# Performance work log

Hardware: AMD Instinct MI355X
Metric: run time of the kernel (lower is better)

Reference implementation:

```python
import jax, jax.numpy as jnp
import numpy as np

U, I, D, K, B, NNEG = 500000, 500000, 64, 32, 8192, 128
W1, W2, W3, W4 = 1e-6, 1.0, 1e-6, 1.0
NEG_WEIGHT, GAMMA, LAMBDA = 200.0, 1e-4, 2.5


def setup_inputs() -> dict:
    key = jax.random.key(0)
    ks = jax.random.split(key, 14)
    return {
        "users": jax.random.randint(ks[0], (B,), 0, U),
        "pos_items": jax.random.randint(ks[1], (B,), 0, I),
        "neg_items": jax.random.randint(ks[2], (B, NNEG), 0, I),
        "rpkms": jax.random.normal(ks[3], (B,), dtype=jnp.float32),
        "user_emb": jax.random.normal(ks[4], (U, D), dtype=jnp.float32) * 1e-2,
        "item_emb": jax.random.normal(ks[5], (I, D), dtype=jnp.float32) * 1e-2,
        "beta_uD": jax.random.uniform(ks[6], (U,), dtype=jnp.float32),
        "beta_iD": jax.random.uniform(ks[7], (I,), dtype=jnp.float32),
        "ii_neighbor_mat": jax.random.randint(ks[8], (I, K), 0, I),
        "ii_constraint_mat": jax.random.uniform(ks[9], (I, K), dtype=jnp.float32),
        "mse_u_w": jax.random.normal(ks[10], (D, D), dtype=jnp.float32) * 0.05,
        "mse_u_b": jnp.zeros((D,), jnp.float32),
        "mse_i_w": jax.random.normal(ks[11], (D, D), dtype=jnp.float32) * 0.05,
        "mse_i_b": jnp.zeros((D,), jnp.float32),
        "fc1_w1": jax.random.normal(ks[12], (D, 2 * D), dtype=jnp.float32) * 0.05,
        "fc1_b1": jnp.zeros((D,), jnp.float32),
        "fc1_w2": jax.random.normal(ks[13], (1, D), dtype=jnp.float32) * 0.05,
        "fc1_b2": jnp.zeros((1,), jnp.float32),
    }


def reference(users, pos_items, neg_items, rpkms, user_emb, item_emb,
              beta_uD, beta_iD, ii_neighbor_mat, ii_constraint_mat,
              mse_u_w, mse_u_b, mse_i_w, mse_i_b,
              fc1_w1, fc1_b1, fc1_w2, fc1_b2):
    sp = jax.nn.softplus  # -log(sigmoid(x)) == softplus(-x)

    ue = user_emb[users]            # [B, D]
    pe = item_emb[pos_items]        # [B, D]
    ne = item_emb[neg_items]        # [B, N, D]

    # ---- omegas ----
    pos_w = W1 + W2 * beta_uD[users] * beta_iD[pos_items]          # [B]
    neg_w = W3 + W4 * beta_uD[users][:, None] * beta_iD[neg_items]  # [B, N]

    # ---- cal_loss_L (weighted BCE with logits) ----
    pos_scores = jnp.sum(ue * pe, axis=-1)                  # [B]
    neg_scores = jnp.einsum('bd,bnd->bn', ue, ne)           # [B, N]
    pos_loss = pos_w * sp(-pos_scores)                      # label 1
    neg_loss = jnp.mean(neg_w * sp(neg_scores), axis=-1)    # label 0, mean over negs
    loss_L = jnp.mean(pos_loss + neg_loss * NEG_WEIGHT)

    # ---- norm_loss over all learned parameters ----
    params = (user_emb, item_emb, mse_u_w, mse_u_b, mse_i_w, mse_i_b,
              fc1_w1, fc1_b1, fc1_w2, fc1_b2)
    norm = GAMMA * 0.5 * sum(jnp.sum(p * p) for p in params)

    # ---- cal_loss_I: gather item-item neighbors of pos_items ----
    nbr = item_emb[ii_neighbor_mat[pos_items]]              # [B, K, D]
    sim = ii_constraint_mat[pos_items]                      # [B, K]
    loss_I = LAMBDA * jnp.mean(sim * sp(-jnp.einsum('bd,bkd->bk', ue, nbr)))

    # ---- mse_loss ----
    feat_u = ue @ mse_u_w.T + mse_u_b
    feat_i = pe @ mse_i_w.T + mse_i_b
    pred = jnp.sum(feat_u * feat_i, axis=-1)
    mse = jnp.mean((pred - rpkms) ** 2)

    total = loss_L + norm + loss_I + mse
    zero = jnp.float32(0.0)  # torch returns torch.tensor(0.0) as 4th element
    return jnp.stack([total, loss_L, loss_I, zero, mse, norm])
```

## Files before the change

kernel.cpp:

```cpp
#include <hip/hip_runtime.h>
#include <math.h>

#define UU 500000
#define II 500000
#define DD 64
#define KK 32
#define BB 8192
#define NNEG 128

#define NORMB 1024
#define GATHB (BB / 4)

typedef float v4f __attribute__((ext_vector_type(4)));

__device__ __forceinline__ float softplus_f(float x) {
    return fmaxf(x, 0.0f) + log1pf(expf(-fabsf(x)));
}

__device__ __forceinline__ float waveReduceSum(float v) {
#pragma unroll
    for (int off = 32; off > 0; off >>= 1) v += __shfl_xor(v, off, 64);
    return v;
}

__global__ __launch_bounds__(256) void fused_kernel(
    const int* __restrict__ users, const int* __restrict__ pos_items,
    const int* __restrict__ neg_items,
    const float* __restrict__ user_emb, const float* __restrict__ item_emb,
    const float* __restrict__ beta_uD, const float* __restrict__ beta_iD,
    const int* __restrict__ ii_nbr, const float* __restrict__ ii_con,
    const float* __restrict__ mse_u_w, const float* __restrict__ mse_u_b,
    const float* __restrict__ mse_i_w, const float* __restrict__ mse_i_b,
    const float* __restrict__ fc1_w1, const float* __restrict__ fc1_b1,
    const float* __restrict__ fc1_w2, const float* __restrict__ fc1_b2,
    float* __restrict__ acc)
{
    const int wave = threadIdx.x >> 6;
    const int lane = threadIdx.x & 63;
    __shared__ float red[4];

    if (blockIdx.x < NORMB) {
        const size_t tid = (size_t)blockIdx.x * blockDim.x + threadIdx.x;
        const size_t st  = (size_t)NORMB * 256;
        const size_t n4  = (size_t)UU * DD / 4;
        float s0 = 0.f, s1 = 0.f, s2 = 0.f, s3 = 0.f;

        {
            const v4f* a = (const v4f*)user_emb;
            size_t i = tid;
            for (; i + 3 * st < n4; i += 4 * st) {
                v4f x0 = __builtin_nontemporal_load(&a[i]);
                v4f x1 = __builtin_nontemporal_load(&a[i + st]);
                v4f x2 = __builtin_nontemporal_load(&a[i + 2 * st]);
                v4f x3 = __builtin_nontemporal_load(&a[i + 3 * st]);
                s0 += x0.x*x0.x + x0.y*x0.y + x0.z*x0.z + x0.w*x0.w;
                s1 += x1.x*x1.x + x1.y*x1.y + x1.z*x1.z + x1.w*x1.w;
                s2 += x2.x*x2.x + x2.y*x2.y + x2.z*x2.z + x2.w*x2.w;
                s3 += x3.x*x3.x + x3.y*x3.y + x3.z*x3.z + x3.w*x3.w;
            }
            for (; i < n4; i += st) {
                v4f x = __builtin_nontemporal_load(&a[i]);
                s0 += x.x*x.x + x.y*x.y + x.z*x.z + x.w*x.w;
            }
        }
        {
            const v4f* c = (const v4f*)item_emb;
            size_t i = tid;
            for (; i + 3 * st < n4; i += 4 * st) {
                v4f x0 = c[i];
                v4f x1 = c[i + st];
                v4f x2 = c[i + 2 * st];
                v4f x3 = c[i + 3 * st];
                s0 += x0.x*x0.x + x0.y*x0.y + x0.z*x0.z + x0.w*x0.w;
                s1 += x1.x*x1.x + x1.y*x1.y + x1.z*x1.z + x1.w*x1.w;
                s2 += x2.x*x2.x + x2.y*x2.y + x2.z*x2.z + x2.w*x2.w;
                s3 += x3.x*x3.x + x3.y*x3.y + x3.z*x3.z + x3.w*x3.w;
            }
            for (; i < n4; i += st) {
                v4f x = c[i];
                s0 += x.x*x.x + x.y*x.y + x.z*x.z + x.w*x.w;
            }
        }
        float s = (s0 + s1) + (s2 + s3);
        for (size_t i = tid; i < (size_t)DD * DD; i += st)
            s += mse_u_w[i] * mse_u_w[i] + mse_i_w[i] * mse_i_w[i];
        for (size_t i = tid; i < (size_t)DD * 2 * DD; i += st)
            s += fc1_w1[i] * fc1_w1[i];
        for (size_t i = tid; i < (size_t)DD; i += st)
            s += mse_u_b[i] * mse_u_b[i] + mse_i_b[i] * mse_i_b[i]
               + fc1_b1[i] * fc1_b1[i] + fc1_w2[i] * fc1_w2[i];
        if (tid == 0) s += fc1_b2[0] * fc1_b2[0];

        s = waveReduceSum(s);
        if (lane == 0) red[wave] = s;
        __syncthreads();
        if (threadIdx.x == 0)
            atomicAdd(&acc[2], red[0] + red[1] + red[2] + red[3]);
        return;
    }

    const int b = (blockIdx.x - NORMB) * 4 + wave;
    float accL = 0.f, accI = 0.f;

    const int u_idx = users[b];
    const int p_idx = pos_items[b];
    const float u_reg = user_emb[(size_t)u_idx * DD + lane];
    const float bu = beta_uD[u_idx];

    __shared__ float sU[4][DD];
    sU[wave][lane] = u_reg;

    const int q  = lane & 3;
    const int li = lane >> 2;

    float4 uv[4];
#pragma unroll
    for (int j = 0; j < 4; ++j)
        uv[j] = *(const float4*)&sU[wave][j * 16 + q * 4];

    {
        const float p = item_emb[(size_t)p_idx * DD + lane];
        const float pos_dot = waveReduceSum(u_reg * p);
        if (lane == 0)
            accL += (1e-6f + bu * beta_iD[p_idx]) * softplus_f(-pos_dot);
    }

    const int i0 = neg_items[(size_t)b * NNEG + lane];
    const int i1 = neg_items[(size_t)b * NNEG + 64 + lane];
    const float bn0 = beta_iD[i0];
    const float bn1 = beta_iD[i1];

    const float negscale4 = 0.25f * (200.0f / (float)NNEG);

#pragma unroll
    for (int g = 0; g < 2; ++g) {
        const int   srcI = g ? i1 : i0;
        const float srcB = g ? bn1 : bn0;
        float4 vb[4][4];
        float  bi4[4];
#pragma unroll
        for (int t = 0; t < 4; ++t) {
            const int n = t * 16 + li;
            const int idx = __shfl(srcI, n, 64);
            bi4[t] = __shfl(srcB, n, 64);
            const float* row = item_emb + (size_t)idx * DD + q * 4;
#pragma unroll
            for (int j = 0; j < 4; ++j)
                vb[t][j] = *(const float4*)(row + j * 16);
        }
#pragma unroll
        for (int t = 0; t < 4; ++t) {
            float dot = 0.f;
#pragma unroll
            for (int j = 0; j < 4; ++j) {
                dot = fmaf(vb[t][j].x, uv[j].x, dot);
                dot = fmaf(vb[t][j].y, uv[j].y, dot);
                dot = fmaf(vb[t][j].z, uv[j].z, dot);
                dot = fmaf(vb[t][j].w, uv[j].w, dot);
            }
            dot += __shfl_xor(dot, 1, 64);
            dot += __shfl_xor(dot, 2, 64);
            accL += negscale4 * (1e-6f + bu * bi4[t]) * softplus_f(dot);
        }
    }

    int nbv = 0; float simv = 0.f;
    if (lane < KK) {
        nbv  = ii_nbr[(size_t)p_idx * KK + lane];
        simv = ii_con[(size_t)p_idx * KK + lane];
    }
    {
        float4 vb[2][4];
        float  sk2[2];
#pragma unroll
        for (int t = 0; t < 2; ++t) {
            const int n = t * 16 + li;
            const int idx = __shfl(nbv, n, 64);
            sk2[t] = __shfl(simv, n, 64);
            const float* row = item_emb + (size_t)idx * DD + q * 4;
#pragma unroll
            for (int j = 0; j < 4; ++j)
                vb[t][j] = *(const float4*)(row + j * 16);
        }
#pragma unroll
        for (int t = 0; t < 2; ++t) {
            float dot = 0.f;
#pragma unroll
            for (int j = 0; j < 4; ++j) {
                dot = fmaf(vb[t][j].x, uv[j].x, dot);
                dot = fmaf(vb[t][j].y, uv[j].y, dot);
                dot = fmaf(vb[t][j].z, uv[j].z, dot);
                dot = fmaf(vb[t][j].w, uv[j].w, dot);
            }
            dot += __shfl_xor(dot, 1, 64);
            dot += __shfl_xor(dot, 2, 64);
            accI += 0.25f * sk2[t] * softplus_f(-dot);
        }
    }

    accL = waveReduceSum(accL);
    accI = waveReduceSum(accI);
    __shared__ float redL[4], redI[4];
    if (lane == 0) { redL[wave] = accL; redI[wave] = accI; }
    __syncthreads();
    if (threadIdx.x == 0) {
        atomicAdd(&acc[0], redL[0] + redL[1] + redL[2] + redL[3]);
        atomicAdd(&acc[1], redI[0] + redI[1] + redI[2] + redI[3]);
    }
}

__global__ __launch_bounds__(256) void mse_kernel(
    const int* __restrict__ users, const int* __restrict__ pos_items,
    const float* __restrict__ rpkms,
    const float* __restrict__ user_emb, const float* __restrict__ item_emb,
    const float* __restrict__ mse_u_w, const float* __restrict__ mse_u_b,
    const float* __restrict__ mse_i_w, const float* __restrict__ mse_i_b,
    float* __restrict__ acc)
{
    __shared__ float sWu[DD * (DD + 1)];
    __shared__ float sWi[DD * (DD + 1)];
    __shared__ float sBu[DD], sBi[DD];
    __shared__ float sUe[4][DD], sPe[4][DD];

    for (int i = threadIdx.x; i < DD * DD; i += blockDim.x) {
        const int r = i >> 6, c = i & 63;
        sWu[r * (DD + 1) + c] = mse_u_w[i];
        sWi[r * (DD + 1) + c] = mse_i_w[i];
    }
    if (threadIdx.x < DD) {
        sBu[threadIdx.x] = mse_u_b[threadIdx.x];
        sBi[threadIdx.x] = mse_i_b[threadIdx.x];
    }

    const int wave = threadIdx.x >> 6;
    const int lane = threadIdx.x & 63;
    const int b = blockIdx.x * 4 + wave;
    sUe[wave][lane] = user_emb[(size_t)users[b] * DD + lane];
    sPe[wave][lane] = item_emb[(size_t)pos_items[b] * DD + lane];
    __syncthreads();

    float fu = sBu[lane];
    float fi = sBi[lane];
#pragma unroll 8
    for (int d = 0; d < DD; ++d) {
        fu += sUe[wave][d] * sWu[lane * (DD + 1) + d];
        fi += sPe[wave][d] * sWi[lane * (DD + 1) + d];
    }
    const float pred = waveReduceSum(fu * fi);
    if (lane == 0) {
        const float diff = pred - rpkms[b];
        atomicAdd(&acc[3], diff * diff);
    }
}

__global__ void finalize_kernel(const float* __restrict__ acc, float* __restrict__ out)
{
    if (threadIdx.x == 0) {
        const float loss_L = acc[0] / (float)BB;
        const float loss_I = 2.5f * acc[1] / (float)(BB * KK);
        const float mse    = acc[3] / (float)BB;
        const float norm   = 1e-4f * 0.5f * acc[2];
        const float total  = loss_L + norm + loss_I + mse;
        out[0] = total;
        out[1] = loss_L;
        out[2] = loss_I;
        out[3] = 0.0f;
        out[4] = mse;
        out[5] = norm;
    }
}

extern "C" void kernel_launch(void* const* d_in, const int* in_sizes, int n_in,
                              void* d_out, int out_size, void* d_ws, size_t ws_size,
                              hipStream_t stream)
{
    const int*   users      = (const int*)  d_in[0];
    const int*   pos_items  = (const int*)  d_in[1];
    const int*   neg_items  = (const int*)  d_in[2];
    const float* rpkms      = (const float*)d_in[3];
    const float* user_emb   = (const float*)d_in[4];
    const float* item_emb   = (const float*)d_in[5];
    const float* beta_uD    = (const float*)d_in[6];
    const float* beta_iD    = (const float*)d_in[7];
    const int*   ii_nbr     = (const int*)  d_in[8];
    const float* ii_con     = (const float*)d_in[9];
    const float* mse_u_w    = (const float*)d_in[10];
    const float* mse_u_b    = (const float*)d_in[11];
    const float* mse_i_w    = (const float*)d_in[12];
    const float* mse_i_b    = (const float*)d_in[13];
    const float* fc1_w1     = (const float*)d_in[14];
    const float* fc1_b1     = (const float*)d_in[15];
    const float* fc1_w2     = (const float*)d_in[16];
    const float* fc1_b2     = (const float*)d_in[17];

    float* acc = (float*)d_ws;
    hipMemsetAsync(d_ws, 0, 4 * sizeof(float), stream);

    fused_kernel<<<NORMB + GATHB, 256, 0, stream>>>(users, pos_items, neg_items,
                                                    user_emb, item_emb, beta_uD, beta_iD,
                                                    ii_nbr, ii_con,
                                                    mse_u_w, mse_u_b, mse_i_w, mse_i_b,
                                                    fc1_w1, fc1_b1, fc1_w2, fc1_b2, acc);

    mse_kernel<<<BB / 4, 256, 0, stream>>>(users, pos_items, rpkms,
                                           user_emb, item_emb,
                                           mse_u_w, mse_u_b, mse_i_w, mse_i_b, acc);

    finalize_kernel<<<1, 64, 0, stream>>>(acc, (float*)d_out);
}
```

Baseline: 531.5 us.

## Gather negatives from a bf16 item table built during the norm pass

```diff
diff --git a/kernel.cpp b/kernel.cpp
--- a/kernel.cpp
+++ b/kernel.cpp
@@ -8,9 +8,6 @@
 #define BB 8192
 #define NNEG 128
 
-#define NORMB 1024
-#define GATHB (BB / 4)
-
 typedef float v4f __attribute__((ext_vector_type(4)));
 
 __device__ __forceinline__ float softplus_f(float x) {
@@ -23,7 +20,225 @@
     return v;
 }
 
-__global__ __launch_bounds__(256) void fused_kernel(
+__device__ __forceinline__ unsigned int bf16pack2(float lo, float hi) {
+    unsigned int ul = __float_as_uint(lo);
+    ul += 0x7FFFu + ((ul >> 16) & 1u);
+    unsigned int uh = __float_as_uint(hi);
+    uh += 0x7FFFu + ((uh >> 16) & 1u);
+    return (ul >> 16) | (uh & 0xFFFF0000u);
+}
+
+__global__ __launch_bounds__(256) void norm_convert_kernel(
+    const float* __restrict__ user_emb, const float* __restrict__ item_emb,
+    unsigned int* __restrict__ bfit,
+    const float* __restrict__ mse_u_w, const float* __restrict__ mse_u_b,
+    const float* __restrict__ mse_i_w, const float* __restrict__ mse_i_b,
+    const float* __restrict__ fc1_w1, const float* __restrict__ fc1_b1,
+    const float* __restrict__ fc1_w2, const float* __restrict__ fc1_b2,
+    float* __restrict__ acc)
+{
+    const size_t tid = (size_t)blockIdx.x * blockDim.x + threadIdx.x;
+    const size_t st  = (size_t)gridDim.x * blockDim.x;
+    float s = 0.f;
+
+    {
+        const size_t npair = (size_t)II * DD / 8;
+        const v4f* it4 = (const v4f*)item_emb;
+        uint4* out4 = (uint4*)bfit;
+        for (size_t k = tid; k < npair; k += st) {
+            v4f a = __builtin_nontemporal_load(&it4[2 * k]);
+            v4f b = __builtin_nontemporal_load(&it4[2 * k + 1]);
+            s += a.x*a.x + a.y*a.y + a.z*a.z + a.w*a.w;
+            s += b.x*b.x + b.y*b.y + b.z*b.z + b.w*b.w;
+            uint4 w;
+            w.x = bf16pack2(a.x, a.y);
+            w.y = bf16pack2(a.z, a.w);
+            w.z = bf16pack2(b.x, b.y);
+            w.w = bf16pack2(b.z, b.w);
+            out4[k] = w;
+        }
+    }
+    {
+        const size_t n4 = (size_t)UU * DD / 4;
+        const v4f* a = (const v4f*)user_emb;
+        for (size_t i = tid; i < n4; i += st) {
+            v4f x = __builtin_nontemporal_load(&a[i]);
+            s += x.x*x.x + x.y*x.y + x.z*x.z + x.w*x.w;
+        }
+    }
+    for (size_t i = tid; i < (size_t)DD * DD; i += st)
+        s += mse_u_w[i] * mse_u_w[i] + mse_i_w[i] * mse_i_w[i];
+    for (size_t i = tid; i < (size_t)DD * 2 * DD; i += st)
+        s += fc1_w1[i] * fc1_w1[i];
+    for (size_t i = tid; i < (size_t)DD; i += st)
+        s += mse_u_b[i] * mse_u_b[i] + mse_i_b[i] * mse_i_b[i]
+           + fc1_b1[i] * fc1_b1[i] + fc1_w2[i] * fc1_w2[i];
+    if (tid == 0) s += fc1_b2[0] * fc1_b2[0];
+
+    s = waveReduceSum(s);
+    __shared__ float red[4];
+    if ((threadIdx.x & 63) == 0) red[threadIdx.x >> 6] = s;
+    __syncthreads();
+    if (threadIdx.x == 0)
+        atomicAdd(&acc[2], red[0] + red[1] + red[2] + red[3]);
+}
+
+__global__ __launch_bounds__(256) void gather_mse_kernel(
+    const int* __restrict__ users, const int* __restrict__ pos_items,
+    const int* __restrict__ neg_items, const float* __restrict__ rpkms,
+    const float* __restrict__ user_emb, const float* __restrict__ item_emb,
+    const unsigned int* __restrict__ bfit,
+    const float* __restrict__ beta_uD, const float* __restrict__ beta_iD,
+    const int* __restrict__ ii_nbr, const float* __restrict__ ii_con,
+    const float* __restrict__ mse_u_w, const float* __restrict__ mse_u_b,
+    const float* __restrict__ mse_i_w, const float* __restrict__ mse_i_b,
+    float* __restrict__ acc)
+{
+    const int wave = threadIdx.x >> 6;
+    const int lane = threadIdx.x & 63;
+    const int b = blockIdx.x * 4 + wave;
+
+    const int u_idx = users[b];
+    const int p_idx = pos_items[b];
+    const float u_reg = user_emb[(size_t)u_idx * DD + lane];
+    const float p_reg = item_emb[(size_t)p_idx * DD + lane];
+    const float bu = beta_uD[u_idx];
+
+    __shared__ float sU[4][DD];
+    __shared__ float sP[4][DD];
+    sU[wave][lane] = u_reg;
+    sP[wave][lane] = p_reg;
+
+    const int q  = lane & 3;
+    const int li = lane >> 2;
+
+    float4 uv[4], pv[4];
+#pragma unroll
+    for (int j = 0; j < 4; ++j) {
+        uv[j] = *(const float4*)&sU[wave][q * 16 + j * 4];
+        pv[j] = *(const float4*)&sP[wave][q * 16 + j * 4];
+    }
+
+    float accL = 0.f, accI = 0.f, accM = 0.f;
+
+    {
+        const float pos_dot = waveReduceSum(u_reg * p_reg);
+        if (lane == 0)
+            accL += (1e-6f + bu * beta_iD[p_idx]) * softplus_f(-pos_dot);
+    }
+
+    const int i0 = neg_items[(size_t)b * NNEG + lane];
+    const int i1 = neg_items[(size_t)b * NNEG + 64 + lane];
+    const float bn0 = beta_iD[i0];
+    const float bn1 = beta_iD[i1];
+    int nbv = 0; float simv = 0.f;
+    if (lane < KK) {
+        nbv  = ii_nbr[(size_t)p_idx * KK + lane];
+        simv = ii_con[(size_t)p_idx * KK + lane];
+    }
+
+    const float negscale4 = 0.25f * (200.0f / (float)NNEG);
+
+    uint4 rg[3][2];
+    float rw[3];
+
+#define PREP(g, slot)                                                          \
+    {                                                                          \
+        int idx; float w;                                                      \
+        if ((g) < 4)      { idx = __shfl(i0, (g) * 16 + li, 64);               \
+                            w   = __shfl(bn0, (g) * 16 + li, 64); }            \
+        else if ((g) < 8) { idx = __shfl(i1, ((g) - 4) * 16 + li, 64);         \
+                            w   = __shfl(bn1, ((g) - 4) * 16 + li, 64); }      \
+        else              { idx = __shfl(nbv, ((g) - 8) * 16 + li, 64);        \
+                            w   = __shfl(simv, ((g) - 8) * 16 + li, 64); }     \
+        const uint4* row = (const uint4*)(bfit + (size_t)idx * (DD / 2));      \
+        rg[slot][0] = row[q * 2];                                              \
+        rg[slot][1] = row[q * 2 + 1];                                          \
+        rw[slot] = w;                                                          \
+    }
+
+#define DOT8(wv, ua, ub, d)                                                    \
+    {                                                                          \
+        d = fmaf(__uint_as_float((wv).x << 16), ua.x, d);                      \
+        d = fmaf(__uint_as_float((wv).x & 0xFFFF0000u), ua.y, d);              \
+        d = fmaf(__uint_as_float((wv).y << 16), ua.z, d);                      \
+        d = fmaf(__uint_as_float((wv).y & 0xFFFF0000u), ua.w, d);              \
+        d = fmaf(__uint_as_float((wv).z << 16), ub.x, d);                      \
+        d = fmaf(__uint_as_float((wv).z & 0xFFFF0000u), ub.y, d);              \
+        d = fmaf(__uint_as_float((wv).w << 16), ub.z, d);                      \
+        d = fmaf(__uint_as_float((wv).w & 0xFFFF0000u), ub.w, d);              \
+    }
+
+#define CONSUME(g, slot)                                                       \
+    {                                                                          \
+        float dot = 0.f;                                                       \
+        DOT8(rg[slot][0], uv[0], uv[1], dot);                                  \
+        DOT8(rg[slot][1], uv[2], uv[3], dot);                                  \
+        dot += __shfl_xor(dot, 1, 64);                                         \
+        dot += __shfl_xor(dot, 2, 64);                                         \
+        if ((g) < 8) accL += negscale4 * (1e-6f + bu * rw[slot]) * softplus_f(dot); \
+        else         accI += 0.25f * rw[slot] * softplus_f(-dot);              \
+    }
+
+    PREP(0, 0); PREP(1, 1); PREP(2, 2);
+    CONSUME(0, 0); PREP(3, 0);
+    CONSUME(1, 1); PREP(4, 1);
+    CONSUME(2, 2); PREP(5, 2);
+    CONSUME(3, 0); PREP(6, 0);
+    CONSUME(4, 1); PREP(7, 1);
+    CONSUME(5, 2); PREP(8, 2);
+    CONSUME(6, 0); PREP(9, 0);
+    CONSUME(7, 1);
+    CONSUME(8, 2);
+    CONSUME(9, 0);
+#undef PREP
+#undef DOT8
+#undef CONSUME
+
+    {
+        float pq = 0.f;
+#pragma unroll
+        for (int g = 0; g < 4; ++g) {
+            const int r = g * 16 + li;
+            const float* wur = mse_u_w + r * DD + q * 16;
+            const float* wir = mse_i_w + r * DD + q * 16;
+            float fu = 0.f, fi = 0.f;
+#pragma unroll
+            for (int j = 0; j < 4; ++j) {
+                const float4 a = *(const float4*)(wur + j * 4);
+                fu = fmaf(a.x, uv[j].x, fu); fu = fmaf(a.y, uv[j].y, fu);
+                fu = fmaf(a.z, uv[j].z, fu); fu = fmaf(a.w, uv[j].w, fu);
+                const float4 c = *(const float4*)(wir + j * 4);
+                fi = fmaf(c.x, pv[j].x, fi); fi = fmaf(c.y, pv[j].y, fi);
+                fi = fmaf(c.z, pv[j].z, fi); fi = fmaf(c.w, pv[j].w, fi);
+            }
+            fu += __shfl_xor(fu, 1, 64); fu += __shfl_xor(fu, 2, 64);
+            fi += __shfl_xor(fi, 1, 64); fi += __shfl_xor(fi, 2, 64);
+            fu += mse_u_b[r];
+            fi += mse_i_b[r];
+            pq += fu * fi;
+        }
+        const float pred = waveReduceSum(pq) * 0.25f;
+        if (lane == 0) {
+            const float diff = pred - rpkms[b];
+            accM += diff * diff;
+        }
+    }
+
+    accL = waveReduceSum(accL);
+    accI = waveReduceSum(accI);
+    __shared__ float redL[4], redI[4], redM[4];
+    if (lane == 0) { redL[wave] = accL; redI[wave] = accI; redM[wave] = accM; }
+    __syncthreads();
+    if (threadIdx.x == 0) {
+        atomicAdd(&acc[0], redL[0] + redL[1] + redL[2] + redL[3]);
+        atomicAdd(&acc[1], redI[0] + redI[1] + redI[2] + redI[3]);
+        atomicAdd(&acc[3], redM[0] + redM[1] + redM[2] + redM[3]);
+    }
+}
+
+#define NORMB 1024
+__global__ __launch_bounds__(256) void fb_fused_kernel(
     const int* __restrict__ users, const int* __restrict__ pos_items,
     const int* __restrict__ neg_items,
     const float* __restrict__ user_emb, const float* __restrict__ item_emb,
@@ -43,45 +258,15 @@
         const size_t tid = (size_t)blockIdx.x * blockDim.x + threadIdx.x;
         const size_t st  = (size_t)NORMB * 256;
         const size_t n4  = (size_t)UU * DD / 4;
-        float s0 = 0.f, s1 = 0.f, s2 = 0.f, s3 = 0.f;
-
-        {
-            const v4f* a = (const v4f*)user_emb;
-            size_t i = tid;
-            for (; i + 3 * st < n4; i += 4 * st) {
-                v4f x0 = __builtin_nontemporal_load(&a[i]);
-                v4f x1 = __builtin_nontemporal_load(&a[i + st]);
-                v4f x2 = __builtin_nontemporal_load(&a[i + 2 * st]);
-                v4f x3 = __builtin_nontemporal_load(&a[i + 3 * st]);
-                s0 += x0.x*x0.x + x0.y*x0.y + x0.z*x0.z + x0.w*x0.w;
-                s1 += x1.x*x1.x + x1.y*x1.y + x1.z*x1.z + x1.w*x1.w;
-                s2 += x2.x*x2.x + x2.y*x2.y + x2.z*x2.z + x2.w*x2.w;
-                s3 += x3.x*x3.x + x3.y*x3.y + x3.z*x3.z + x3.w*x3.w;
-            }
-            for (; i < n4; i += st) {
-                v4f x = __builtin_nontemporal_load(&a[i]);
-                s0 += x.x*x.x + x.y*x.y + x.z*x.z + x.w*x.w;
-            }
-        }
-        {
-            const v4f* c = (const v4f*)item_emb;
-            size_t i = tid;
-            for (; i + 3 * st < n4; i += 4 * st) {
-                v4f x0 = c[i];
-                v4f x1 = c[i + st];
-                v4f x2 = c[i + 2 * st];
-                v4f x3 = c[i + 3 * st];
-                s0 += x0.x*x0.x + x0.y*x0.y + x0.z*x0.z + x0.w*x0.w;
-                s1 += x1.x*x1.x + x1.y*x1.y + x1.z*x1.z + x1.w*x1.w;
-                s2 += x2.x*x2.x + x2.y*x2.y + x2.z*x2.z + x2.w*x2.w;
-                s3 += x3.x*x3.x + x3.y*x3.y + x3.z*x3.z + x3.w*x3.w;
-            }
-            for (; i < n4; i += st) {
-                v4f x = c[i];
-                s0 += x.x*x.x + x.y*x.y + x.z*x.z + x.w*x.w;
-            }
-        }
-        float s = (s0 + s1) + (s2 + s3);
+        float s = 0.f;
+        const v4f* a = (const v4f*)user_emb;
+        for (size_t i = tid; i < n4; i += st) {
+            v4f x = a[i]; s += x.x*x.x + x.y*x.y + x.z*x.z + x.w*x.w;
+        }
+        const v4f* c = (const v4f*)item_emb;
+        for (size_t i = tid; i < n4; i += st) {
+            v4f x = c[i]; s += x.x*x.x + x.y*x.y + x.z*x.z + x.w*x.w;
+        }
         for (size_t i = tid; i < (size_t)DD * DD; i += st)
             s += mse_u_w[i] * mse_u_w[i] + mse_i_w[i] * mse_i_w[i];
         for (size_t i = tid; i < (size_t)DD * 2 * DD; i += st)
@@ -90,7 +275,6 @@
             s += mse_u_b[i] * mse_u_b[i] + mse_i_b[i] * mse_i_b[i]
                + fc1_b1[i] * fc1_b1[i] + fc1_w2[i] * fc1_w2[i];
         if (tid == 0) s += fc1_b2[0] * fc1_b2[0];
-
         s = waveReduceSum(s);
         if (lane == 0) red[wave] = s;
         __syncthreads();
@@ -101,43 +285,32 @@
 
     const int b = (blockIdx.x - NORMB) * 4 + wave;
     float accL = 0.f, accI = 0.f;
-
     const int u_idx = users[b];
     const int p_idx = pos_items[b];
     const float u_reg = user_emb[(size_t)u_idx * DD + lane];
     const float bu = beta_uD[u_idx];
-
     __shared__ float sU[4][DD];
     sU[wave][lane] = u_reg;
-
     const int q  = lane & 3;
     const int li = lane >> 2;
-
     float4 uv[4];
 #pragma unroll
-    for (int j = 0; j < 4; ++j)
-        uv[j] = *(const float4*)&sU[wave][j * 16 + q * 4];
-
+    for (int j = 0; j < 4; ++j) uv[j] = *(const float4*)&sU[wave][j * 16 + q * 4];
     {
         const float p = item_emb[(size_t)p_idx * DD + lane];
         const float pos_dot = waveReduceSum(u_reg * p);
-        if (lane == 0)
-            accL += (1e-6f + bu * beta_iD[p_idx]) * softplus_f(-pos_dot);
-    }
-
+        if (lane == 0) accL += (1e-6f + bu * beta_iD[p_idx]) * softplus_f(-pos_dot);
+    }
     const int i0 = neg_items[(size_t)b * NNEG + lane];
     const int i1 = neg_items[(size_t)b * NNEG + 64 + lane];
     const float bn0 = beta_iD[i0];
     const float bn1 = beta_iD[i1];
-
     const float negscale4 = 0.25f * (200.0f / (float)NNEG);
-
 #pragma unroll
     for (int g = 0; g < 2; ++g) {
         const int   srcI = g ? i1 : i0;
         const float srcB = g ? bn1 : bn0;
-        float4 vb[4][4];
-        float  bi4[4];
+        float4 vb[4][4]; float bi4[4];
 #pragma unroll
         for (int t = 0; t < 4; ++t) {
             const int n = t * 16 + li;
@@ -145,8 +318,7 @@
             bi4[t] = __shfl(srcB, n, 64);
             const float* row = item_emb + (size_t)idx * DD + q * 4;
 #pragma unroll
-            for (int j = 0; j < 4; ++j)
-                vb[t][j] = *(const float4*)(row + j * 16);
+            for (int j = 0; j < 4; ++j) vb[t][j] = *(const float4*)(row + j * 16);
         }
 #pragma unroll
         for (int t = 0; t < 4; ++t) {
@@ -163,15 +335,13 @@
             accL += negscale4 * (1e-6f + bu * bi4[t]) * softplus_f(dot);
         }
     }
-
     int nbv = 0; float simv = 0.f;
     if (lane < KK) {
         nbv  = ii_nbr[(size_t)p_idx * KK + lane];
         simv = ii_con[(size_t)p_idx * KK + lane];
     }
     {
-        float4 vb[2][4];
-        float  sk2[2];
+        float4 vb[2][4]; float sk2[2];
 #pragma unroll
         for (int t = 0; t < 2; ++t) {
             const int n = t * 16 + li;
@@ -179,8 +349,7 @@
             sk2[t] = __shfl(simv, n, 64);
             const float* row = item_emb + (size_t)idx * DD + q * 4;
 #pragma unroll
-            for (int j = 0; j < 4; ++j)
-                vb[t][j] = *(const float4*)(row + j * 16);
+            for (int j = 0; j < 4; ++j) vb[t][j] = *(const float4*)(row + j * 16);
         }
 #pragma unroll
         for (int t = 0; t < 2; ++t) {
@@ -197,7 +366,6 @@
             accI += 0.25f * sk2[t] * softplus_f(-dot);
         }
     }
-
     accL = waveReduceSum(accL);
     accI = waveReduceSum(accI);
     __shared__ float redL[4], redI[4];
@@ -209,7 +377,7 @@
     }
 }
 
-__global__ __launch_bounds__(256) void mse_kernel(
+__global__ __launch_bounds__(256) void fb_mse_kernel(
     const int* __restrict__ users, const int* __restrict__ pos_items,
     const float* __restrict__ rpkms,
     const float* __restrict__ user_emb, const float* __restrict__ item_emb,
@@ -221,7 +389,6 @@
     __shared__ float sWi[DD * (DD + 1)];
     __shared__ float sBu[DD], sBi[DD];
     __shared__ float sUe[4][DD], sPe[4][DD];
-
     for (int i = threadIdx.x; i < DD * DD; i += blockDim.x) {
         const int r = i >> 6, c = i & 63;
         sWu[r * (DD + 1) + c] = mse_u_w[i];
@@ -231,14 +398,12 @@
         sBu[threadIdx.x] = mse_u_b[threadIdx.x];
         sBi[threadIdx.x] = mse_i_b[threadIdx.x];
     }
-
     const int wave = threadIdx.x >> 6;
     const int lane = threadIdx.x & 63;
     const int b = blockIdx.x * 4 + wave;
     sUe[wave][lane] = user_emb[(size_t)users[b] * DD + lane];
     sPe[wave][lane] = item_emb[(size_t)pos_items[b] * DD + lane];
     __syncthreads();
-
     float fu = sBu[lane];
     float fi = sBi[lane];
 #pragma unroll 8
@@ -296,15 +461,29 @@
     float* acc = (float*)d_ws;
     hipMemsetAsync(d_ws, 0, 4 * sizeof(float), stream);
 
-    fused_kernel<<<NORMB + GATHB, 256, 0, stream>>>(users, pos_items, neg_items,
-                                                    user_emb, item_emb, beta_uD, beta_iD,
-                                                    ii_nbr, ii_con,
-                                                    mse_u_w, mse_u_b, mse_i_w, mse_i_b,
-                                                    fc1_w1, fc1_b1, fc1_w2, fc1_b2, acc);
-
-    mse_kernel<<<BB / 4, 256, 0, stream>>>(users, pos_items, rpkms,
-                                           user_emb, item_emb,
-                                           mse_u_w, mse_u_b, mse_i_w, mse_i_b, acc);
+    const size_t bf_bytes = (size_t)II * DD * 2;
+    const size_t need = 256 + bf_bytes;
+
+    if (ws_size >= need) {
+        unsigned int* bfit = (unsigned int*)((char*)d_ws + 256);
+        norm_convert_kernel<<<4096, 256, 0, stream>>>(
+            user_emb, item_emb, bfit,
+            mse_u_w, mse_u_b, mse_i_w, mse_i_b,
+            fc1_w1, fc1_b1, fc1_w2, fc1_b2, acc);
+        gather_mse_kernel<<<BB / 4, 256, 0, stream>>>(
+            users, pos_items, neg_items, rpkms,
+            user_emb, item_emb, bfit, beta_uD, beta_iD,
+            ii_nbr, ii_con, mse_u_w, mse_u_b, mse_i_w, mse_i_b, acc);
+    } else {
+        fb_fused_kernel<<<NORMB + BB / 4, 256, 0, stream>>>(
+            users, pos_items, neg_items,
+            user_emb, item_emb, beta_uD, beta_iD, ii_nbr, ii_con,
+            mse_u_w, mse_u_b, mse_i_w, mse_i_b,
+            fc1_w1, fc1_b1, fc1_w2, fc1_b2, acc);
+        fb_mse_kernel<<<BB / 4, 256, 0, stream>>>(
+            users, pos_items, rpkms, user_emb, item_emb,
+            mse_u_w, mse_u_b, mse_i_w, mse_i_b, acc);
+    }
 
     finalize_kernel<<<1, 64, 0, stream>>>(acc, (float*)d_out);
 }
```

After: 476.8 us. 10.3% less time.
